# Kernel optimization log

Hardware: AMD Instinct MI355X
Metric: run time of the kernel (lower is better)

Reference implementation:

```python
import jax, jax.numpy as jnp
import numpy as np

NUM_CLASSES = 100000
FEAT_DIM = 128
BATCH = 1024


def setup_inputs() -> dict:
    key = jax.random.key(0)
    k1, k2, k3 = jax.random.split(key, 3)
    x = jax.random.normal(k1, (BATCH, FEAT_DIM), dtype=jnp.float32)
    labels = jax.random.randint(k2, (BATCH,), 0, NUM_CLASSES, dtype=jnp.int64)
    centers = jax.random.normal(k3, (NUM_CLASSES, FEAT_DIM), dtype=jnp.float32)
    return {"x": x, "labels": labels, "centers": centers}


def reference(x, labels, centers):
    # dense (B, C) squared-distance matrix, as in the torch addmm path
    x_sq = jnp.sum(x * x, axis=1, keepdims=True)            # (B, 1)
    c_sq = jnp.sum(centers * centers, axis=1)               # (C,)
    distmat = x_sq + c_sq[None, :] - 2.0 * (x @ centers.T)  # (B, C)
    classes = jnp.arange(centers.shape[0])
    mask = (labels[:, None] == classes[None, :]).astype(distmat.dtype)
    # reduction='mean' averages over the full B*C matrix (torch .mean())
    loss = jnp.mean(distmat * mask)
    return loss
```

## Files before the change

kernel.cpp:

```cpp
#include <hip/hip_runtime.h>

#define BATCH 1024
#define FEAT_DIM 128
#define NUM_CLASSES 100000
#define NBLK 32
#define NTHREADS 1024

__global__ __launch_bounds__(NTHREADS) void centerloss_fused(
    const float* __restrict__ x,
    const int* __restrict__ labels,
    const float* __restrict__ centers,
    float* partial,
    unsigned* cnt,
    float* out) {

    const int wave = threadIdx.x >> 6;
    const int lane = threadIdx.x & 63;
    const int row0 = blockIdx.x * 32 + wave * 2;

    const long long l0 = (long long)labels[row0];
    const long long l1 = (long long)labels[row0 + 1];

    const float2 xa = reinterpret_cast<const float2*>(x)[(long long)row0 * 64 + lane];
    const float2 xb = reinterpret_cast<const float2*>(x)[(long long)(row0 + 1) * 64 + lane];
    const float2 ca = reinterpret_cast<const float2*>(centers)[l0 * 64 + lane];
    const float2 cb = reinterpret_cast<const float2*>(centers)[l1 * 64 + lane];

    const float d0 = xa.x - ca.x, d1 = xa.y - ca.y;
    const float d2 = xb.x - cb.x, d3 = xb.y - cb.y;
    float s = (d0 * d0 + d1 * d1) + (d2 * d2 + d3 * d3);

    #pragma unroll
    for (int o = 32; o > 0; o >>= 1)
        s += __shfl_down(s, o, 64);

    __shared__ float wsum[16];
    __shared__ unsigned old_s;
    if (lane == 0)
        wsum[wave] = s;
    __syncthreads();

    if (threadIdx.x < 64) {
        float p = (lane < 16) ? wsum[lane] : 0.0f;
        #pragma unroll
        for (int o = 8; o > 0; o >>= 1)
            p += __shfl_down(p, o, 64);
        if (lane == 0) {
            __hip_atomic_store(&partial[blockIdx.x], p, __ATOMIC_RELAXED,
                               __HIP_MEMORY_SCOPE_AGENT);
            old_s = __hip_atomic_fetch_add(cnt, 1u, __ATOMIC_ACQ_REL,
                                           __HIP_MEMORY_SCOPE_AGENT);
        }
    }
    __syncthreads();

    if ((old_s & (NBLK - 1)) != (NBLK - 1)) return;

    __builtin_amdgcn_fence(__ATOMIC_ACQUIRE, "agent");
    if (threadIdx.x < 64) {
        float p = (lane < NBLK)
                      ? __hip_atomic_load(&partial[lane], __ATOMIC_RELAXED,
                                          __HIP_MEMORY_SCOPE_AGENT)
                      : 0.0f;
        #pragma unroll
        for (int o = 16; o > 0; o >>= 1)
            p += __shfl_down(p, o, 64);
        if (lane == 0)
            out[0] = p * (1.0f / ((float)BATCH * (float)NUM_CLASSES));
    }
}

extern "C" void kernel_launch(void* const* d_in, const int* in_sizes, int n_in,
                              void* d_out, int out_size, void* d_ws, size_t ws_size,
                              hipStream_t stream) {
    const float* x       = (const float*)d_in[0];
    const int*   labels  = (const int*)d_in[1];
    const float* centers = (const float*)d_in[2];
    float*       out     = (float*)d_out;
    float*       partial = (float*)d_ws;
    unsigned*    cnt     = (unsigned*)((char*)d_ws + 4096);

    centerloss_fused<<<NBLK, NTHREADS, 0, stream>>>(x, labels, centers,
                                                    partial, cnt, out);
}
```

Measured before the change: 10.20 us.

## Use float4 loads with four rows per thread and fewer blocks

Reworks the work split so each thread loads four float4 slices of x and the matching center rows, and the grid drops from 32 to 8 blocks. The final cross-block reduction is shortened to match. This is meant to raise memory-level parallelism per thread, widen each load, and cut the cost of block scheduling and the atomic completion counter. In exchange, fewer CUs are active, which may limit aggregate bandwidth on the gathered center rows.

```diff
diff --git a/kernel.cpp b/kernel.cpp
--- a/kernel.cpp
+++ b/kernel.cpp
@@ -3,7 +3,7 @@
 #define BATCH 1024
 #define FEAT_DIM 128
 #define NUM_CLASSES 100000
-#define NBLK 32
+#define NBLK 8
 #define NTHREADS 1024
 
 __global__ __launch_bounds__(NTHREADS) void centerloss_fused(
@@ -16,19 +16,37 @@
 
     const int wave = threadIdx.x >> 6;
     const int lane = threadIdx.x & 63;
-    const int row0 = blockIdx.x * 32 + wave * 2;
 
-    const long long l0 = (long long)labels[row0];
-    const long long l1 = (long long)labels[row0 + 1];
+    const float4* x4 = reinterpret_cast<const float4*>(x);
+    const float4* c4 = reinterpret_cast<const float4*>(centers);
 
-    const float2 xa = reinterpret_cast<const float2*>(x)[(long long)row0 * 64 + lane];
-    const float2 xb = reinterpret_cast<const float2*>(x)[(long long)(row0 + 1) * 64 + lane];
-    const float2 ca = reinterpret_cast<const float2*>(centers)[l0 * 64 + lane];
-    const float2 cb = reinterpret_cast<const float2*>(centers)[l1 * 64 + lane];
+    const int c0 = blockIdx.x * 4096 + threadIdx.x;
+    const int c1 = c0 + 1024;
+    const int c2 = c0 + 2048;
+    const int c3 = c0 + 3072;
 
-    const float d0 = xa.x - ca.x, d1 = xa.y - ca.y;
-    const float d2 = xb.x - cb.x, d3 = xb.y - cb.y;
-    float s = (d0 * d0 + d1 * d1) + (d2 * d2 + d3 * d3);
+    const long long l0 = (long long)labels[c0 >> 5];
+    const long long l1 = (long long)labels[c1 >> 5];
+    const long long l2 = (long long)labels[c2 >> 5];
+    const long long l3 = (long long)labels[c3 >> 5];
+
+    const float4 xa = x4[c0], xb = x4[c1], xc = x4[c2], xd = x4[c3];
+    const float4 ca = c4[l0 * 32 + (c0 & 31)];
+    const float4 cb = c4[l1 * 32 + (c1 & 31)];
+    const float4 cc = c4[l2 * 32 + (c2 & 31)];
+    const float4 cd = c4[l3 * 32 + (c3 & 31)];
+
+    float s;
+    {
+        const float a0 = xa.x - ca.x, a1 = xa.y - ca.y, a2 = xa.z - ca.z, a3 = xa.w - ca.w;
+        const float b0 = xb.x - cb.x, b1 = xb.y - cb.y, b2 = xb.z - cb.z, b3 = xb.w - cb.w;
+        const float g0 = xc.x - cc.x, g1 = xc.y - cc.y, g2 = xc.z - cc.z, g3 = xc.w - cc.w;
+        const float h0 = xd.x - cd.x, h1 = xd.y - cd.y, h2 = xd.z - cd.z, h3 = xd.w - cd.w;
+        s = (((a0 * a0 + a1 * a1) + (a2 * a2 + a3 * a3))
+           + ((b0 * b0 + b1 * b1) + (b2 * b2 + b3 * b3)))
+          + (((g0 * g0 + g1 * g1) + (g2 * g2 + g3 * g3))
+           + ((h0 * h0 + h1 * h1) + (h2 * h2 + h3 * h3)));
+    }
 
     #pragma unroll
     for (int o = 32; o > 0; o >>= 1)
@@ -63,7 +81,7 @@
                                           __HIP_MEMORY_SCOPE_AGENT)
                       : 0.0f;
         #pragma unroll
-        for (int o = 16; o > 0; o >>= 1)
+        for (int o = 4; o > 0; o >>= 1)
             p += __shfl_down(p, o, 64);
         if (lane == 0)
             out[0] = p * (1.0f / ((float)BATCH * (float)NUM_CLASSES));
```

Result: slower. 11.04 us (+8.3%).
